# Performance work log

Hardware: AMD Instinct MI355X
Metric: run time of the kernel (lower is better)

The kernel has to match this reference:

```python
import jax, jax.numpy as jnp
import numpy as np

B, N, D = 16, 1024, 128


def setup_inputs() -> dict:
    key = jax.random.key(0)
    ks = jax.random.split(key, 12)
    x = jax.random.normal(ks[0], (B, N, D), dtype=jnp.float32)
    # binary symmetric-ish adjacency mask (0/1 floats)
    adj = jax.random.randint(ks[1], (B, N, N), 0, 2).astype(jnp.float32)
    Ww = jax.random.normal(ks[2], (D, D), dtype=jnp.float32) * 0.05
    Wb = jax.random.normal(ks[3], (D,), dtype=jnp.float32) * 0.05
    A = jax.random.normal(ks[4], (D, D), dtype=jnp.float32) * 0.05
    wi_u = jax.random.normal(ks[5], (D,), dtype=jnp.float32) * 0.05
    wi_x = jax.random.normal(ks[6], (D,), dtype=jnp.float32) * 0.05
    wf_u = jax.random.normal(ks[7], (D,), dtype=jnp.float32) * 0.05
    wf_x = jax.random.normal(ks[8], (D,), dtype=jnp.float32) * 0.05
    wo_u = jax.random.normal(ks[9], (D,), dtype=jnp.float32) * 0.05
    wo_x = jax.random.normal(ks[10], (D,), dtype=jnp.float32) * 0.05
    return {"x": x, "adj": adj, "Ww": Ww, "Wb": Wb, "A": A,
            "wi_u": wi_u, "wi_x": wi_x, "wf_u": wf_u, "wf_x": wf_x,
            "wo_u": wo_u, "wo_x": wo_x}


def reference(x, adj, Ww, Wb, A, wi_u, wi_x, wf_u, wf_x, wo_u, wo_x):
    # h = W(x): [B,N,D]
    h = jnp.einsum('bnf,df->bnd', x, Ww) + Wb
    # e[b,j,k] = (h A) . h  -> symmetrized dense scores [B,N,N]
    e = jnp.einsum('bjl,bkl->bjk', jnp.einsum('bjd,dl->bjl', h, A), h)
    e = e + jnp.swapaxes(e, 1, 2)
    # masked softmax over axis=1 (columns), then re-mask by adj
    scores = jnp.where(adj > 0, e, 0.0)
    attention = jax.nn.softmax(scores, axis=1) * adj
    # aggregation
    h_prime = jax.nn.relu(jnp.einsum('bij,bjk->bik', attention, h))
    # LSTM-style gates: scalar per node, broadcast over features
    ic = jax.nn.sigmoid(h_prime @ wi_u + x @ wi_x)[..., None]
    fc = jax.nn.sigmoid(h_prime @ wf_u + x @ wf_x)[..., None]
    oc = jax.nn.sigmoid(h_prime @ wo_u + x @ wo_x)[..., None]
    return oc * jnp.tanh(ic * h_prime + fc * x)
```

## Files before the change

### kernel.cpp

```cpp
#include <hip/hip_runtime.h>


#define B_ 16
#define N_ 1024
#define D_ 128

typedef __attribute__((ext_vector_type(8))) short bf16x8;
typedef __attribute__((ext_vector_type(4))) float f32x4;

__device__ __forceinline__ float b2f(unsigned short u) {
    union { unsigned int i; float f; } v; v.i = ((unsigned int)u) << 16; return v.f;
}
__device__ __forceinline__ unsigned short f2b(float f) {
    union { float f; unsigned int i; } v; v.f = f;
    unsigned int x = v.i;
    return (unsigned short)((x + 0x7fffu + ((x >> 16) & 1u)) >> 16);
}
__device__ __forceinline__ float clamp60(float v) {
    return fminf(fmaxf(v, -60.f), 60.f);
}
__device__ __forceinline__ bf16x8 load8f(const float* p) {
    float4 a = *reinterpret_cast<const float4*>(p);
    float4 b = *reinterpret_cast<const float4*>(p + 4);
    bf16x8 v;
    v[0] = (short)f2b(a.x); v[1] = (short)f2b(a.y);
    v[2] = (short)f2b(a.z); v[3] = (short)f2b(a.w);
    v[4] = (short)f2b(b.x); v[5] = (short)f2b(b.y);
    v[6] = (short)f2b(b.z); v[7] = (short)f2b(b.w);
    return v;
}

__global__ __launch_bounds__(256) void k0_w2t(
    const float* __restrict__ Ww, const float* __restrict__ Wb,
    const float* __restrict__ A, unsigned short* __restrict__ WwB,
    unsigned short* __restrict__ W2T, float* __restrict__ wbA) {
    int t = blockIdx.x * 256 + threadIdx.x;
    int l = t >> 7, f = t & 127;
    float acc = 0.f;
    for (int d = 0; d < 128; ++d)
        acc += A[d * 128 + l] * Ww[d * 128 + f];
    W2T[l * 128 + f] = f2b(acc);
    WwB[t] = f2b(Ww[t]);
    if (blockIdx.x == 0 && threadIdx.x < 128) {
        float s = 0.f;
        for (int d = 0; d < 128; ++d) s += Wb[d] * A[d * 128 + threadIdx.x];
        wbA[threadIdx.x] = s;
    }
}

__global__ __launch_bounds__(256) void kmask(
    const float* __restrict__ adj, unsigned long long* __restrict__ maskJ) {
    int w = threadIdx.x >> 6, lane = threadIdx.x & 63;
    size_t base = ((size_t)blockIdx.x * 4 + w) * 256;
    unsigned long long w0 = __ballot(adj[base + 0 * 64 + lane] > 0.f);
    unsigned long long w1 = __ballot(adj[base + 1 * 64 + lane] > 0.f);
    unsigned long long w2 = __ballot(adj[base + 2 * 64 + lane] > 0.f);
    unsigned long long w3 = __ballot(adj[base + 3 * 64 + lane] > 0.f);
    unsigned long long o = lane == 0 ? w0 : lane == 1 ? w1 : lane == 2 ? w2 : w3;
    if (lane < 4) maskJ[(base >> 6) + lane] = o;
}

__global__ __launch_bounds__(256) void k1_hu(
    const float* __restrict__ x, const unsigned short* __restrict__ WwB,
    const float* __restrict__ Wb, const unsigned short* __restrict__ W2T,
    const float* __restrict__ wbA,
    unsigned short* __restrict__ h, unsigned short* __restrict__ u,
    unsigned short* __restrict__ hT) {
    __shared__ unsigned short lds[16][128];
    int w = threadIdx.x >> 6, lane = threadIdx.x & 63;
    int c = lane & 15, q = lane >> 4;
    int rowbase = blockIdx.x * 16;
    int b = rowbase >> 10;
    int n0 = rowbase & 1023;
    bf16x8 xa[4];
    const float* xrow = x + (size_t)(rowbase + c) * 128;
#pragma unroll
    for (int ks = 0; ks < 4; ++ks)
        xa[ks] = load8f(xrow + ks * 32 + q * 8);
#pragma unroll
    for (int tt = 0; tt < 2; ++tt) {
        int t = w * 2 + tt;
        f32x4 acch = {0.f, 0.f, 0.f, 0.f};
        f32x4 accu = {0.f, 0.f, 0.f, 0.f};
        const unsigned short* wwrow = WwB + (t * 16 + c) * 128;
        const unsigned short* w2row = W2T + (t * 16 + c) * 128;
#pragma unroll
        for (int ks = 0; ks < 4; ++ks) {
            bf16x8 bw = *reinterpret_cast<const bf16x8*>(wwrow + ks * 32 + q * 8);
            bf16x8 b2 = *reinterpret_cast<const bf16x8*>(w2row + ks * 32 + q * 8);
            acch = __builtin_amdgcn_mfma_f32_16x16x32_bf16(xa[ks], bw, acch, 0, 0, 0);
            accu = __builtin_amdgcn_mfma_f32_16x16x32_bf16(xa[ks], b2, accu, 0, 0, 0);
        }
        float wb = Wb[t * 16 + c];
        float ub = wbA[t * 16 + c];
#pragma unroll
        for (int r = 0; r < 4; ++r) {
            int row = rowbase + q * 4 + r;
            unsigned short hv = f2b(acch[r] + wb);
            unsigned short uv = f2b(accu[r] + ub);
            h[(size_t)row * 128 + t * 16 + c] = hv;
            u[(size_t)row * 128 + t * 16 + c] = uv;
            lds[q * 4 + r][t * 16 + c] = hv;
        }
    }
    __syncthreads();
    int tid = threadIdx.x;
    if (tid < 128) {
        int d = tid;
        unsigned int p[8];
#pragma unroll
        for (int k = 0; k < 8; ++k) {
            unsigned int v0 = lds[2 * k][d], v1 = lds[2 * k + 1][d];
            p[k] = v0 | (v1 << 16);
        }
        size_t basehT = ((size_t)(b * 128 + d)) * 1024 + n0;
        uint4* dst = reinterpret_cast<uint4*>(hT + basehT);
        dst[0] = make_uint4(p[0], p[1], p[2], p[3]);
        dst[1] = make_uint4(p[4], p[5], p[6], p[7]);
    }
}

__global__ __launch_bounds__(256) void k2_scores(
    const unsigned short* __restrict__ h, const unsigned short* __restrict__ u,
    const unsigned long long* __restrict__ maskJ,
    unsigned short* __restrict__ att, float* __restrict__ colpart) {
    __shared__ unsigned long long lmask[32][16];
    __shared__ __align__(16) unsigned short stage[4][32][40];
    int w = threadIdx.x >> 6, lane = threadIdx.x & 63;
    int c = lane & 15, q = lane >> 4;
    int b = blockIdx.x >> 5;
    int iblk = blockIdx.x & 31;
    int i0 = iblk * 32;
    const unsigned short* hb = h + (size_t)b * N_ * D_;
    const unsigned short* ub = u + (size_t)b * N_ * D_;

    {
        int tid = threadIdx.x;
        lmask[tid >> 4][tid & 15] =
            maskJ[(size_t)(b * 1024 + i0 + (tid >> 4)) * 16 + (tid & 15)];
        lmask[16 + (tid >> 4)][tid & 15] =
            maskJ[(size_t)(b * 1024 + i0 + 16 + (tid >> 4)) * 16 + (tid & 15)];
    }
    __syncthreads();

    bf16x8 Au0[4], Ah0[4], Au1[4], Ah1[4];
#pragma unroll
    for (int ks = 0; ks < 4; ++ks) {
        Au0[ks] = *reinterpret_cast<const bf16x8*>(ub + (i0 + c) * 128 + ks * 32 + q * 8);
        Ah0[ks] = *reinterpret_cast<const bf16x8*>(hb + (i0 + c) * 128 + ks * 32 + q * 8);
        Au1[ks] = *reinterpret_cast<const bf16x8*>(ub + (i0 + 16 + c) * 128 + ks * 32 + q * 8);
        Ah1[ks] = *reinterpret_cast<const bf16x8*>(hb + (i0 + 16 + c) * 128 + ks * 32 + q * 8);
    }
    unsigned short* attrow = att + ((size_t)(b * 1024 + i0)) * 1024;
    float* cprow = colpart + ((size_t)(b * 32 + iblk)) * 1024;

    int jt0 = w * 16;
#pragma unroll
    for (int p = 0; p < 8; ++p) {
        int jt = jt0 + p * 2;
        int j0 = jt * 16;
        bf16x8 Bh[2][4], Bu[2][4];
#pragma unroll
        for (int s = 0; s < 2; ++s)
#pragma unroll
            for (int ks = 0; ks < 4; ++ks) {
                Bh[s][ks] = *reinterpret_cast<const bf16x8*>(
                    hb + (j0 + s * 16 + c) * 128 + ks * 32 + q * 8);
                Bu[s][ks] = *reinterpret_cast<const bf16x8*>(
                    ub + (j0 + s * 16 + c) * 128 + ks * 32 + q * 8);
            }
        f32x4 acc[2][2][2];
#pragma unroll
        for (int g = 0; g < 2; ++g)
#pragma unroll
            for (int s = 0; s < 2; ++s)
#pragma unroll
                for (int pr = 0; pr < 2; ++pr)
                    acc[g][s][pr] = (f32x4){0.f, 0.f, 0.f, 0.f};
#pragma unroll
        for (int ks = 0; ks < 4; ++ks) {
            acc[0][0][0] = __builtin_amdgcn_mfma_f32_16x16x32_bf16(Au0[ks], Bh[0][ks], acc[0][0][0], 0, 0, 0);
            acc[0][0][1] = __builtin_amdgcn_mfma_f32_16x16x32_bf16(Ah0[ks], Bu[0][ks], acc[0][0][1], 0, 0, 0);
            acc[1][0][0] = __builtin_amdgcn_mfma_f32_16x16x32_bf16(Au1[ks], Bh[0][ks], acc[1][0][0], 0, 0, 0);
            acc[1][0][1] = __builtin_amdgcn_mfma_f32_16x16x32_bf16(Ah1[ks], Bu[0][ks], acc[1][0][1], 0, 0, 0);
            acc[0][1][0] = __builtin_amdgcn_mfma_f32_16x16x32_bf16(Au0[ks], Bh[1][ks], acc[0][1][0], 0, 0, 0);
            acc[0][1][1] = __builtin_amdgcn_mfma_f32_16x16x32_bf16(Ah0[ks], Bu[1][ks], acc[0][1][1], 0, 0, 0);
            acc[1][1][0] = __builtin_amdgcn_mfma_f32_16x16x32_bf16(Au1[ks], Bh[1][ks], acc[1][1][0], 0, 0, 0);
            acc[1][1][1] = __builtin_amdgcn_mfma_f32_16x16x32_bf16(Ah1[ks], Bu[1][ks], acc[1][1][1], 0, 0, 0);
        }
        float colpA = 0.f, colpB = 0.f;
#pragma unroll
        for (int s = 0; s < 2; ++s) {
            int jts = jt + s;
            int wd = jts >> 2, sh = (jts & 3) * 16;
#pragma unroll
            for (int g = 0; g < 2; ++g)
#pragma unroll
                for (int r = 0; r < 4; ++r) {
                    float e = acc[g][s][0][r] + acc[g][s][1][r];
                    int row = g * 16 + q * 4 + r;
                    bool m = (lmask[row][wd] >> (sh + c)) & 1ull;
                    float ex = m ? __expf(clamp60(e)) : 0.f;
                    float cadd = m ? ex : 1.0f;
                    if (s == 0) colpA += cadd; else colpB += cadd;
                    stage[w][row][s * 16 + c] = f2b(ex);
                }
        }
        colpA += __shfl_xor(colpA, 16, 64);
        colpA += __shfl_xor(colpA, 32, 64);
        colpB += __shfl_xor(colpB, 16, 64);
        colpB += __shfl_xor(colpB, 32, 64);
        if (q == 0) {
            cprow[j0 + c] = colpA;
            cprow[j0 + 16 + c] = colpB;
        }
        int row2 = lane & 31, half = lane >> 5;
        const uint4* sp = reinterpret_cast<const uint4*>(&stage[w][row2][half * 16]);
        uint4 v0 = sp[0], v1 = sp[1];
        uint4* gp = reinterpret_cast<uint4*>(attrow + (size_t)row2 * 1024 + j0 + half * 16);
        gp[0] = v0; gp[1] = v1;
    }
}

__global__ __launch_bounds__(256) void k2b_recip(
    const float* __restrict__ colpart, float* __restrict__ rl0) {
    int g = blockIdx.x * 256 + threadIdx.x;
    int b = g >> 10, j = g & 1023;
    float s = 0.f;
    const float* p = colpart + (size_t)b * 32 * 1024 + j;
    for (int ib = 0; ib < 32; ++ib) s += p[(size_t)ib * 1024];
    rl0[g] = 1.0f / s;
}

__global__ __launch_bounds__(256) void k3_gemm(
    const unsigned short* __restrict__ att, const float* __restrict__ rl0,
    const unsigned short* __restrict__ hT, const float* __restrict__ x,
    const float* __restrict__ wi_u, const float* __restrict__ wi_x,
    const float* __restrict__ wf_u, const float* __restrict__ wf_x,
    const float* __restrict__ wo_u, const float* __restrict__ wo_x,
    float* __restrict__ out) {
    __shared__ __align__(16) unsigned short smem[16384];
    int w = threadIdx.x >> 6, lane = threadIdx.x & 63;
    int c = lane & 15, q = lane >> 4;
    int b = blockIdx.x >> 6;
    int i0 = (blockIdx.x & 63) * 16;

    const char* attblk = reinterpret_cast<const char*>(att + ((size_t)(b * 1024 + i0)) * 1024);
#pragma unroll
    for (int it = 0; it < 8; ++it) {
        int L = it * 4096 + w * 1024;
        int row = L >> 11;
        int swz = (row & 7) << 4;
        int cb = (L & 2047) + lane * 16;
        const char* src = attblk + (row << 11) + (cb ^ swz);
        unsigned short* dst = smem + (L >> 1);
        __builtin_amdgcn_global_load_lds(
            (const __attribute__((address_space(1))) unsigned int*)(const void*)src,
            (__attribute__((address_space(3))) unsigned int*)(void*)dst, 16, 0, 0);
    }
    __syncthreads();

    int t0 = w * 2, t1 = t0 + 1;
    const unsigned short* hTb = hT + (size_t)b * 128 * 1024;
    const unsigned short* bt0p = hTb + (size_t)(t0 * 16 + c) * 1024 + q * 8;
    const unsigned short* bt1p = hTb + (size_t)(t1 * 16 + c) * 1024 + q * 8;
    const float* rl0p = rl0 + b * 1024 + q * 8;
    const char* avbase = reinterpret_cast<const char*>(smem) + c * 2048;
    int swzc = (c & 7) << 4;
    int offq = q * 16;

    f32x4 acc0 = {0.f, 0.f, 0.f, 0.f};
    f32x4 acc1 = {0.f, 0.f, 0.f, 0.f};
#pragma unroll 4
    for (int jp = 0; jp < 32; ++jp) {
        bf16x8 eraw = *reinterpret_cast<const bf16x8*>(
            avbase + (((jp << 6) + offq) ^ swzc));
        float4 r0 = *reinterpret_cast<const float4*>(rl0p + jp * 32);
        float4 r1 = *reinterpret_cast<const float4*>(rl0p + jp * 32 + 4);
        bf16x8 av;
        av[0] = (short)f2b(b2f((unsigned short)eraw[0]) * r0.x);
        av[1] = (short)f2b(b2f((unsigned short)eraw[1]) * r0.y);
        av[2] = (short)f2b(b2f((unsigned short)eraw[2]) * r0.z);
        av[3] = (short)f2b(b2f((unsigned short)eraw[3]) * r0.w);
        av[4] = (short)f2b(b2f((unsigned short)eraw[4]) * r1.x);
        av[5] = (short)f2b(b2f((unsigned short)eraw[5]) * r1.y);
        av[6] = (short)f2b(b2f((unsigned short)eraw[6]) * r1.z);
        av[7] = (short)f2b(b2f((unsigned short)eraw[7]) * r1.w);
        bf16x8 b0 = *reinterpret_cast<const bf16x8*>(bt0p + jp * 32);
        bf16x8 b1 = *reinterpret_cast<const bf16x8*>(bt1p + jp * 32);
        acc0 = __builtin_amdgcn_mfma_f32_16x16x32_bf16(av, b0, acc0, 0, 0, 0);
        acc1 = __builtin_amdgcn_mfma_f32_16x16x32_bf16(av, b1, acc1, 0, 0, 0);
    }

    float hp[2][4], xv[2][4];
    const float* xb = x + ((size_t)(b * 1024 + i0)) * 128;
#pragma unroll
    for (int r = 0; r < 4; ++r) {
        hp[0][r] = fmaxf(acc0[r], 0.f);
        hp[1][r] = fmaxf(acc1[r], 0.f);
        xv[0][r] = xb[(size_t)(q * 4 + r) * 128 + t0 * 16 + c];
        xv[1][r] = xb[(size_t)(q * 4 + r) * 128 + t1 * 16 + c];
    }
    float wiu[2], wix[2], wfu[2], wfx[2], wou[2], wox[2];
#pragma unroll
    for (int tt = 0; tt < 2; ++tt) {
        int d = (t0 + tt) * 16 + c;
        wiu[tt] = wi_u[d]; wix[tt] = wi_x[d];
        wfu[tt] = wf_u[d]; wfx[tt] = wf_x[d];
        wou[tt] = wo_u[d]; wox[tt] = wo_x[d];
    }
    float zi[4], zf[4], zo[4];
#pragma unroll
    for (int r = 0; r < 4; ++r) {
        zi[r] = hp[0][r] * wiu[0] + hp[1][r] * wiu[1]
              + xv[0][r] * wix[0] + xv[1][r] * wix[1];
        zf[r] = hp[0][r] * wfu[0] + hp[1][r] * wfu[1]
              + xv[0][r] * wfx[0] + xv[1][r] * wfx[1];
        zo[r] = hp[0][r] * wou[0] + hp[1][r] * wou[1]
              + xv[0][r] * wox[0] + xv[1][r] * wox[1];
        zi[r] += __shfl_xor(zi[r], 1, 64); zi[r] += __shfl_xor(zi[r], 2, 64);
        zi[r] += __shfl_xor(zi[r], 4, 64); zi[r] += __shfl_xor(zi[r], 8, 64);
        zf[r] += __shfl_xor(zf[r], 1, 64); zf[r] += __shfl_xor(zf[r], 2, 64);
        zf[r] += __shfl_xor(zf[r], 4, 64); zf[r] += __shfl_xor(zf[r], 8, 64);
        zo[r] += __shfl_xor(zo[r], 1, 64); zo[r] += __shfl_xor(zo[r], 2, 64);
        zo[r] += __shfl_xor(zo[r], 4, 64); zo[r] += __shfl_xor(zo[r], 8, 64);
    }
    __syncthreads();
    float* gp = reinterpret_cast<float*>(smem);
    if (c == 0) {
#pragma unroll
        for (int r = 0; r < 4; ++r) {
            int row = q * 4 + r;
            gp[(w * 16 + row) * 4 + 0] = zi[r];
            gp[(w * 16 + row) * 4 + 1] = zf[r];
            gp[(w * 16 + row) * 4 + 2] = zo[r];
        }
    }
    __syncthreads();
#pragma unroll
    for (int r = 0; r < 4; ++r) {
        int row = q * 4 + r;
        float Zi = gp[(0 * 16 + row) * 4 + 0] + gp[(1 * 16 + row) * 4 + 0]
                 + gp[(2 * 16 + row) * 4 + 0] + gp[(3 * 16 + row) * 4 + 0];
        float Zf = gp[(0 * 16 + row) * 4 + 1] + gp[(1 * 16 + row) * 4 + 1]
                 + gp[(2 * 16 + row) * 4 + 1] + gp[(3 * 16 + row) * 4 + 1];
        float Zo = gp[(0 * 16 + row) * 4 + 2] + gp[(1 * 16 + row) * 4 + 2]
                 + gp[(2 * 16 + row) * 4 + 2] + gp[(3 * 16 + row) * 4 + 2];
        float ic = 1.f / (1.f + __expf(-Zi));
        float fc = 1.f / (1.f + __expf(-Zf));
        float oc = 1.f / (1.f + __expf(-Zo));
#pragma unroll
        for (int tt = 0; tt < 2; ++tt) {
            float zz = ic * hp[tt][r] + fc * xv[tt][r];
            float th = 1.f - 2.f / (__expf(2.f * zz) + 1.f);
            out[(size_t)(b * 1024 + i0 + row) * 128 + (t0 + tt) * 16 + c] = oc * th;
        }
    }
}

extern "C" void kernel_launch(void* const* d_in, const int* in_sizes, int n_in,
                              void* d_out, int out_size, void* d_ws, size_t ws_size,
                              hipStream_t stream) {
    const float* x    = (const float*)d_in[0];
    const float* adj  = (const float*)d_in[1];
    const float* Ww   = (const float*)d_in[2];
    const float* Wb   = (const float*)d_in[3];
    const float* A    = (const float*)d_in[4];
    const float* wi_u = (const float*)d_in[5];
    const float* wi_x = (const float*)d_in[6];
    const float* wf_u = (const float*)d_in[7];
    const float* wf_x = (const float*)d_in[8];
    const float* wo_u = (const float*)d_in[9];
    const float* wo_x = (const float*)d_in[10];
    float* out = (float*)d_out;
    char* ws = (char*)d_ws;

    if (ws_size >= (56ull << 20)) {
        unsigned short* WwB = (unsigned short*)(ws);
        unsigned short* W2T = (unsigned short*)(ws + (32u << 10));
        float* wbA          = (float*)(ws + (64u << 10));
        float* rl0          = (float*)(ws + (128u << 10));
        unsigned long long* maskJ = (unsigned long long*)(ws + (256u << 10));
        float* colpart      = (float*)(ws + (4ull << 20));
        unsigned short* h   = (unsigned short*)(ws + (8ull << 20));
        unsigned short* u   = (unsigned short*)(ws + (12ull << 20));
        unsigned short* hT  = (unsigned short*)(ws + (16ull << 20));
        unsigned short* att = (unsigned short*)(ws + (20ull << 20));

        k0_w2t<<<64, 256, 0, stream>>>(Ww, Wb, A, WwB, W2T, wbA);
        kmask<<<16384, 256, 0, stream>>>(adj, maskJ);
        k1_hu<<<1024, 256, 0, stream>>>(x, WwB, Wb, W2T, wbA, h, u, hT);
        k2_scores<<<512, 256, 0, stream>>>(h, u, maskJ, att, colpart);
        k2b_recip<<<64, 256, 0, stream>>>(colpart, rl0);
        k3_gemm<<<1024, 256, 0, stream>>>(att, rl0, hT, x,
                                          wi_u, wi_x, wf_u, wf_x, wo_u, wo_x, out);
    } else {
        unsigned short* WwB = (unsigned short*)(ws);
        unsigned short* W2T = (unsigned short*)(ws + (32u << 10));
        float* wbA          = (float*)(ws + (64u << 10));
        float* rl0          = (float*)(ws + (128u << 10));
        unsigned long long* maskJ = (unsigned long long*)(ws + (256u << 10));
        float* colpart      = (float*)(ws + (3ull << 20));
        unsigned short* h   = (unsigned short*)(ws + (5ull << 20));
        unsigned short* u   = (unsigned short*)(ws + (9ull << 20));
        unsigned short* hT  = (unsigned short*)(ws + (13ull << 20));
        unsigned short* att = (unsigned short*)(ws + (17ull << 20));

        k0_w2t<<<64, 256, 0, stream>>>(Ww, Wb, A, WwB, W2T, wbA);
        kmask<<<16384, 256, 0, stream>>>(adj, maskJ);
        k1_hu<<<1024, 256, 0, stream>>>(x, WwB, Wb, W2T, wbA, h, u, hT);
        k2_scores<<<512, 256, 0, stream>>>(h, u, maskJ, att, colpart);
        k2b_recip<<<64, 256, 0, stream>>>(colpart, rl0);
        k3_gemm<<<1024, 256, 0, stream>>>(att, rl0, hT, x,
                                          wi_u, wi_x, wf_u, wf_x, wo_u, wo_x, out);
    }
}
```

Measured before the change: 225.2 us.

## Split score kernel across column halves and load attention directly in aggregation GEMM

The score kernel now launches twice as many blocks, each covering half of the column tiles, to raise occupancy and parallelism. Each block still loads the same row-side operands and mask, so those loads are repeated across the two halves. The aggregation kernel drops its LDS staging of the attention tile via global_load_lds and the barrier that followed it, and reads attention rows straight from global memory. It also splits the MFMA accumulation into four independent chains, which breaks the serial dependency at the cost of extra registers and a final sum.

After: 239.9 us. 6.5% more time.

```diff
diff --git a/kernel.cpp b/kernel.cpp
--- a/kernel.cpp
+++ b/kernel.cpp
@@ -128,8 +128,9 @@
     __shared__ __align__(16) unsigned short stage[4][32][40];
     int w = threadIdx.x >> 6, lane = threadIdx.x & 63;
     int c = lane & 15, q = lane >> 4;
-    int b = blockIdx.x >> 5;
-    int iblk = blockIdx.x & 31;
+    int b = blockIdx.x >> 6;
+    int iblk = (blockIdx.x >> 1) & 31;
+    int jh = blockIdx.x & 1;
     int i0 = iblk * 32;
     const unsigned short* hb = h + (size_t)b * N_ * D_;
     const unsigned short* ub = u + (size_t)b * N_ * D_;
@@ -154,9 +155,9 @@
     unsigned short* attrow = att + ((size_t)(b * 1024 + i0)) * 1024;
     float* cprow = colpart + ((size_t)(b * 32 + iblk)) * 1024;
 
-    int jt0 = w * 16;
-#pragma unroll
-    for (int p = 0; p < 8; ++p) {
+    int jt0 = jh * 32 + w * 8;
+#pragma unroll
+    for (int p = 0; p < 4; ++p) {
         int jt = jt0 + p * 2;
         int j0 = jt * 16;
         bf16x8 Bh[2][4], Bu[2][4];
@@ -239,42 +240,28 @@
     const float* __restrict__ wf_u, const float* __restrict__ wf_x,
     const float* __restrict__ wo_u, const float* __restrict__ wo_x,
     float* __restrict__ out) {
-    __shared__ __align__(16) unsigned short smem[16384];
+    __shared__ float gred[4][16][4];
     int w = threadIdx.x >> 6, lane = threadIdx.x & 63;
     int c = lane & 15, q = lane >> 4;
     int b = blockIdx.x >> 6;
     int i0 = (blockIdx.x & 63) * 16;
 
-    const char* attblk = reinterpret_cast<const char*>(att + ((size_t)(b * 1024 + i0)) * 1024);
-#pragma unroll
-    for (int it = 0; it < 8; ++it) {
-        int L = it * 4096 + w * 1024;
-        int row = L >> 11;
-        int swz = (row & 7) << 4;
-        int cb = (L & 2047) + lane * 16;
-        const char* src = attblk + (row << 11) + (cb ^ swz);
-        unsigned short* dst = smem + (L >> 1);
-        __builtin_amdgcn_global_load_lds(
-            (const __attribute__((address_space(1))) unsigned int*)(const void*)src,
-            (__attribute__((address_space(3))) unsigned int*)(void*)dst, 16, 0, 0);
-    }
-    __syncthreads();
-
     int t0 = w * 2, t1 = t0 + 1;
+    const unsigned short* attrow = att + ((size_t)(b * 1024 + i0 + c)) * 1024 + q * 8;
     const unsigned short* hTb = hT + (size_t)b * 128 * 1024;
     const unsigned short* bt0p = hTb + (size_t)(t0 * 16 + c) * 1024 + q * 8;
     const unsigned short* bt1p = hTb + (size_t)(t1 * 16 + c) * 1024 + q * 8;
     const float* rl0p = rl0 + b * 1024 + q * 8;
-    const char* avbase = reinterpret_cast<const char*>(smem) + c * 2048;
-    int swzc = (c & 7) << 4;
-    int offq = q * 16;
-
-    f32x4 acc0 = {0.f, 0.f, 0.f, 0.f};
-    f32x4 acc1 = {0.f, 0.f, 0.f, 0.f};
-#pragma unroll 4
+
+    f32x4 acc0[4], acc1[4];
+#pragma unroll
+    for (int ch = 0; ch < 4; ++ch) {
+        acc0[ch] = (f32x4){0.f, 0.f, 0.f, 0.f};
+        acc1[ch] = (f32x4){0.f, 0.f, 0.f, 0.f};
+    }
+#pragma unroll
     for (int jp = 0; jp < 32; ++jp) {
-        bf16x8 eraw = *reinterpret_cast<const bf16x8*>(
-            avbase + (((jp << 6) + offq) ^ swzc));
+        bf16x8 eraw = *reinterpret_cast<const bf16x8*>(attrow + jp * 32);
         float4 r0 = *reinterpret_cast<const float4*>(rl0p + jp * 32);
         float4 r1 = *reinterpret_cast<const float4*>(rl0p + jp * 32 + 4);
         bf16x8 av;
@@ -288,16 +275,16 @@
         av[7] = (short)f2b(b2f((unsigned short)eraw[7]) * r1.w);
         bf16x8 b0 = *reinterpret_cast<const bf16x8*>(bt0p + jp * 32);
         bf16x8 b1 = *reinterpret_cast<const bf16x8*>(bt1p + jp * 32);
-        acc0 = __builtin_amdgcn_mfma_f32_16x16x32_bf16(av, b0, acc0, 0, 0, 0);
-        acc1 = __builtin_amdgcn_mfma_f32_16x16x32_bf16(av, b1, acc1, 0, 0, 0);
+        acc0[jp >> 3] = __builtin_amdgcn_mfma_f32_16x16x32_bf16(av, b0, acc0[jp >> 3], 0, 0, 0);
+        acc1[jp >> 3] = __builtin_amdgcn_mfma_f32_16x16x32_bf16(av, b1, acc1[jp >> 3], 0, 0, 0);
     }
 
     float hp[2][4], xv[2][4];
     const float* xb = x + ((size_t)(b * 1024 + i0)) * 128;
 #pragma unroll
     for (int r = 0; r < 4; ++r) {
-        hp[0][r] = fmaxf(acc0[r], 0.f);
-        hp[1][r] = fmaxf(acc1[r], 0.f);
+        hp[0][r] = fmaxf(((acc0[0][r] + acc0[1][r]) + acc0[2][r]) + acc0[3][r], 0.f);
+        hp[1][r] = fmaxf(((acc1[0][r] + acc1[1][r]) + acc1[2][r]) + acc1[3][r], 0.f);
         xv[0][r] = xb[(size_t)(q * 4 + r) * 128 + t0 * 16 + c];
         xv[1][r] = xb[(size_t)(q * 4 + r) * 128 + t1 * 16 + c];
     }
@@ -325,27 +312,25 @@
         zo[r] += __shfl_xor(zo[r], 1, 64); zo[r] += __shfl_xor(zo[r], 2, 64);
         zo[r] += __shfl_xor(zo[r], 4, 64); zo[r] += __shfl_xor(zo[r], 8, 64);
     }
-    __syncthreads();
-    float* gp = reinterpret_cast<float*>(smem);
     if (c == 0) {
 #pragma unroll
         for (int r = 0; r < 4; ++r) {
             int row = q * 4 + r;
-            gp[(w * 16 + row) * 4 + 0] = zi[r];
-            gp[(w * 16 + row) * 4 + 1] = zf[r];
-            gp[(w * 16 + row) * 4 + 2] = zo[r];
+            gred[w][row][0] = zi[r];
+            gred[w][row][1] = zf[r];
+            gred[w][row][2] = zo[r];
         }
     }
     __syncthreads();
 #pragma unroll
     for (int r = 0; r < 4; ++r) {
         int row = q * 4 + r;
-        float Zi = gp[(0 * 16 + row) * 4 + 0] + gp[(1 * 16 + row) * 4 + 0]
-                 + gp[(2 * 16 + row) * 4 + 0] + gp[(3 * 16 + row) * 4 + 0];
-        float Zf = gp[(0 * 16 + row) * 4 + 1] + gp[(1 * 16 + row) * 4 + 1]
-                 + gp[(2 * 16 + row) * 4 + 1] + gp[(3 * 16 + row) * 4 + 1];
-        float Zo = gp[(0 * 16 + row) * 4 + 2] + gp[(1 * 16 + row) * 4 + 2]
-                 + gp[(2 * 16 + row) * 4 + 2] + gp[(3 * 16 + row) * 4 + 2];
+        float Zi = gred[0][row][0] + gred[1][row][0]
+                 + gred[2][row][0] + gred[3][row][0];
+        float Zf = gred[0][row][1] + gred[1][row][1]
+                 + gred[2][row][1] + gred[3][row][1];
+        float Zo = gred[0][row][2] + gred[1][row][2]
+                 + gred[2][row][2] + gred[3][row][2];
         float ic = 1.f / (1.f + __expf(-Zi));
         float fc = 1.f / (1.f + __expf(-Zf));
         float oc = 1.f / (1.f + __expf(-Zo));
@@ -390,7 +375,7 @@
         k0_w2t<<<64, 256, 0, stream>>>(Ww, Wb, A, WwB, W2T, wbA);
         kmask<<<16384, 256, 0, stream>>>(adj, maskJ);
         k1_hu<<<1024, 256, 0, stream>>>(x, WwB, Wb, W2T, wbA, h, u, hT);
-        k2_scores<<<512, 256, 0, stream>>>(h, u, maskJ, att, colpart);
+        k2_scores<<<1024, 256, 0, stream>>>(h, u, maskJ, att, colpart);
         k2b_recip<<<64, 256, 0, stream>>>(colpart, rl0);
         k3_gemm<<<1024, 256, 0, stream>>>(att, rl0, hT, x,
                                           wi_u, wi_x, wf_u, wf_x, wo_u, wo_x, out);
@@ -409,7 +394,7 @@
         k0_w2t<<<64, 256, 0, stream>>>(Ww, Wb, A, WwB, W2T, wbA);
         kmask<<<16384, 256, 0, stream>>>(adj, maskJ);
         k1_hu<<<1024, 256, 0, stream>>>(x, WwB, Wb, W2T, wbA, h, u, hT);
-        k2_scores<<<512, 256, 0, stream>>>(h, u, maskJ, att, colpart);
+        k2_scores<<<1024, 256, 0, stream>>>(h, u, maskJ, att, colpart);
         k2b_recip<<<64, 256, 0, stream>>>(colpart, rl0);
         k3_gemm<<<1024, 256, 0, stream>>>(att, rl0, hT, x,
                                           wi_u, wi_x, wf_u, wf_x, wo_u, wo_x, out);
```
